# Performance work log

Hardware: AMD Instinct MI355X
Metric: run time of the kernel (lower is better)

Reference implementation:

```python
import jax, jax.numpy as jnp
import numpy as np

TOP_K = 2
EPS = 1e-10


def setup_inputs() -> dict:
    key = jax.random.key(0)
    k1, k2, k3, k4 = jax.random.split(key, 4)
    B, S, H, E = 4, 2048, 1024, 8
    tokens = jax.random.normal(k1, (B, S, H), dtype=jnp.float32)
    router_w = jax.random.normal(k2, (E, H), dtype=jnp.float32) * (1.0 / np.sqrt(H))
    router_b = jax.random.normal(k3, (E,), dtype=jnp.float32) * 0.01
    expert_weights = jax.random.normal(k4, (E, H, H), dtype=jnp.float32) * (1.0 / np.sqrt(H))
    return {"tokens": tokens, "router_w": router_w, "router_b": router_b,
            "expert_weights": expert_weights}


def reference(tokens, router_w, router_b, expert_weights):
    B, S, H = tokens.shape
    E = expert_weights.shape[0]
    # Router (torch Linear: x @ W^T + b)
    logits = jnp.einsum('bsh,eh->bse', tokens, router_w) + router_b  # [B,S,E]
    probs = jax.nn.softmax(logits, axis=-1)
    top_p, top_i = jax.lax.top_k(probs, TOP_K)            # [B,S,K]
    w = top_p / (jnp.sum(top_p, axis=-1, keepdims=True) + EPS)  # normalized weights

    x = tokens.reshape(-1, H)                              # [N,H]
    idx = top_i.reshape(-1, TOP_K)                         # [N,K]
    wf = w.reshape(-1, TOP_K)                              # [N,K]

    # Expert GEMM: compute all experts then gather selected (dense, vectorized
    # equivalent of the sort/pad/grouped-GEMM dispatch; padded rows with
    # original_indices==-1 never contribute to the output).
    y_all = jnp.einsum('nh,ehd->ned', x, expert_weights)   # [N,E,H]
    y_k = jnp.take_along_axis(y_all, idx[:, :, None], axis=1)  # [N,K,H]

    out = jnp.einsum('nk,nkh->nh', wf, y_k)                # weighted combine
    acc = jnp.clip(jnp.sum(wf, axis=-1), EPS, None)        # weight accumulator
    out = (out / acc[:, None]).reshape(B, S, H)

    # epsilon scale tying output to normalized router probs (gradient path)
    scale = 1.0 + jnp.sum(w, axis=-1, keepdims=True) * EPS  # [B,S,1]
    return out * scale
```

## Files before the change

kernel.cpp:

```cpp
#include <hip/hip_runtime.h>
#include <stdint.h>

#define N_TOK 8192
#define H_DIM 1024
#define N_EXP 8
#define GEMM_GRID 1056

typedef __bf16 bf16x8 __attribute__((ext_vector_type(8)));
typedef float floatx4 __attribute__((ext_vector_type(4)));

typedef __attribute__((address_space(1))) void GV;
typedef __attribute__((address_space(3))) void LV;

static __device__ __forceinline__ unsigned short f2b(float f) {
    union { float f; unsigned int i; } v; v.f = f;
    unsigned int u = v.i;
    return (unsigned short)((u + 0x7FFFu + ((u >> 16) & 1u)) >> 16);
}
static __device__ __forceinline__ float b2f(unsigned short u) {
    union { unsigned int i; float f; } v; v.i = ((unsigned int)u) << 16; return v.f;
}

__global__ __launch_bounds__(256) void k_front(
    const float* __restrict__ tokens,
    const float* __restrict__ router_w,
    const float* __restrict__ router_b,
    const float* __restrict__ W,
    int* __restrict__ sel, float* __restrict__ w_arr,
    unsigned short* __restrict__ tokb,
    unsigned short* __restrict__ Bp)
{
    const int t = threadIdx.x;

    if (blockIdx.x >= 2048) {
        const int idx = blockIdx.x - 2048;
        const int kg = idx & 127;
        const int e  = idx >> 7;
        const int d  = t * 4;
        const float* src = W + ((size_t)e * H_DIM + kg * 8) * H_DIM + d;
        float col[8][4];
#pragma unroll
        for (int j = 0; j < 8; ++j) {
            float4 v = *(const float4*)(src + (size_t)j * H_DIM);
            col[j][0] = v.x; col[j][1] = v.y; col[j][2] = v.z; col[j][3] = v.w;
        }
        unsigned short* dst = Bp + ((size_t)(e * 128 + kg) * H_DIM + d) * 8;
#pragma unroll
        for (int k = 0; k < 4; ++k) {
            unsigned short v[8];
#pragma unroll
            for (int j = 0; j < 8; ++j) v[j] = f2b(col[j][k]);
            *(uint4*)(dst + (size_t)k * 8) = *(uint4*)v;
        }
        return;
    }

    const int wave = t >> 6;
    const int lane = t & 63;
    const int n = blockIdx.x * 4 + wave;

    const float* xp = tokens + (size_t)n * H_DIM + lane * 16;
    float x[16];
#pragma unroll
    for (int i = 0; i < 4; ++i) {
        float4 v = *(const float4*)(xp + i * 4);
        x[i * 4 + 0] = v.x; x[i * 4 + 1] = v.y; x[i * 4 + 2] = v.z; x[i * 4 + 3] = v.w;
    }

    {
        unsigned short xb[16];
#pragma unroll
        for (int j = 0; j < 16; ++j) xb[j] = f2b(x[j]);
        unsigned short* dp = tokb + (size_t)n * H_DIM + lane * 16;
        *(uint4*)(dp)     = *(uint4*)(xb);
        *(uint4*)(dp + 8) = *(uint4*)(xb + 8);
    }

    float acc[N_EXP];
#pragma unroll
    for (int e = 0; e < N_EXP; ++e) {
        const float* wp = router_w + e * H_DIM + lane * 16;
        float s = 0.f;
#pragma unroll
        for (int i = 0; i < 4; ++i) {
            float4 v = *(const float4*)(wp + i * 4);
            s += x[i * 4 + 0] * v.x + x[i * 4 + 1] * v.y
               + x[i * 4 + 2] * v.z + x[i * 4 + 3] * v.w;
        }
        acc[e] = s;
    }

#pragma unroll
    for (int e = 0; e < N_EXP; ++e) {
        float a = acc[e];
#pragma unroll
        for (int off = 32; off > 0; off >>= 1) a += __shfl_xor(a, off);
        acc[e] = a;
    }

    if (lane == 0) {
        float lg[N_EXP];
#pragma unroll
        for (int e = 0; e < N_EXP; ++e) lg[e] = acc[e] + router_b[e];
        int e0 = 0;
#pragma unroll
        for (int e = 1; e < N_EXP; ++e) if (lg[e] > lg[e0]) e0 = e;
        int e1 = -1;
#pragma unroll
        for (int e = 0; e < N_EXP; ++e) {
            if (e == e0) continue;
            if (e1 < 0 || lg[e] > lg[e1]) e1 = e;
        }
        float w0 = 1.f / (1.f + __expf(lg[e1] - lg[e0]));
        float w1 = 1.f - w0;
        sel[n] = e0 | (e1 << 4);
        w_arr[n * 2] = w0;
        w_arr[n * 2 + 1] = w1;
    }
}

__global__ __launch_bounds__(256) void k_scan(
    const int* __restrict__ sel, int* __restrict__ cnt, int* __restrict__ bucket)
{
    __shared__ int ssel[N_TOK + N_TOK / 32];
    __shared__ int sc[256];
    const int e = blockIdx.x;
    const int t = threadIdx.x;
#pragma unroll
    for (int i = 0; i < 32; ++i) {
        int n = i * 256 + t;
        ssel[n + (n >> 5)] = sel[n];
    }
    __syncthreads();
    const int base = t * 32;
    int c = 0;
#pragma unroll
    for (int i = 0; i < 32; ++i) {
        int n = base + i;
        int s = ssel[n + (n >> 5)];
        c += ((s & 15) == e) + (((s >> 4) & 15) == e);
    }
    sc[t] = c;
    __syncthreads();
    for (int off = 1; off < 256; off <<= 1) {
        int v = (t >= off) ? sc[t - off] : 0;
        __syncthreads();
        sc[t] += v;
        __syncthreads();
    }
    int pos = sc[t] - c;
    if (t == 255) cnt[e] = sc[255];
#pragma unroll
    for (int i = 0; i < 32; ++i) {
        int n = base + i;
        int s = ssel[n + (n >> 5)];
        if ((s & 15) == e)        bucket[e * N_TOK + pos++] = 2 * n;
        if (((s >> 4) & 15) == e) bucket[e * N_TOK + pos++] = 2 * n + 1;
    }
}

__global__ __launch_bounds__(128, 3) void k_gemm(
    const unsigned short* __restrict__ tokb,
    const unsigned short* __restrict__ Bp,
    const int* __restrict__ cnt, const int* __restrict__ bucket,
    unsigned short* __restrict__ Y)
{
    __shared__ __align__(16) unsigned short Asm[64 * 64];
    __shared__ __align__(16) unsigned short Bsm[8 * 128 * 8];

    const int t = threadIdx.x;
    const int wv = t >> 6, lane = t & 63;
    const int m_lane = lane & 15, quad = lane >> 4;
    const int p_sw = (lane & 7) ^ ((lane >> 3) & 7);

    int cs[N_EXP];
#pragma unroll
    for (int ee = 0; ee < N_EXP; ++ee) cs[ee] = cnt[ee];
    int n_t64 = 0;
#pragma unroll
    for (int ee = 0; ee < N_EXP; ++ee) n_t64 += (cs[ee] + 63) >> 6;
    const int n_it = n_t64 * 8;

    for (int item = blockIdx.x; item < n_it; item += GEMM_GRID) {
        const int t64 = item >> 3;
        const int nt  = item & 7;
        int base = 0, e = 0, mt = 0;
#pragma unroll
        for (int ee = 0; ee < N_EXP; ++ee) {
            int te = (cs[ee] + 63) >> 6;
            if (t64 >= base && t64 < base + te) { e = ee; mt = t64 - base; }
            base += te;
        }
        const int cnt_local = cs[e] - mt * 64;
        const int d0 = nt * 128;
        const int* bk = bucket + e * N_TOK + mt * 64;

        const unsigned short* aptr[4];
#pragma unroll
        for (int i = 0; i < 4; ++i) {
            int r = i * 16 + wv * 8 + (lane >> 3);
            int rid = (r < cnt_local) ? bk[r] : -1;
            int tok = (rid >= 0) ? (rid >> 1) : 0;
            aptr[i] = tokb + (size_t)tok * H_DIM + p_sw * 8;
        }
        const unsigned short* bbase = Bp
            + ((size_t)(e * 128) * H_DIM + d0 + wv * 64 + lane) * 8;

        floatx4 acc[4][4];
#pragma unroll
        for (int i = 0; i < 4; ++i)
#pragma unroll
            for (int j = 0; j < 4; ++j) acc[i][j] = (floatx4){0.f, 0.f, 0.f, 0.f};

        for (int kt = 0; kt < H_DIM / 64; ++kt) {
#pragma unroll
            for (int i = 0; i < 4; ++i)
                __builtin_amdgcn_global_load_lds(
                    (GV*)(aptr[i] + kt * 64),
                    (LV*)(&Asm[i * 1024 + wv * 512]), 16, 0, 0);
#pragma unroll
            for (int i = 0; i < 8; ++i)
                __builtin_amdgcn_global_load_lds(
                    (GV*)(bbase + (size_t)(kt * 8 + i) * (H_DIM * 8)),
                    (LV*)(&Bsm[i * 1024 + wv * 512]), 16, 0, 0);
            __syncthreads();

#pragma unroll
            for (int s = 0; s < 2; ++s) {
                bf16x8 a[4], b[4];
#pragma unroll
                for (int i = 0; i < 4; ++i) {
                    int row = i * 16 + m_lane;
                    a[i] = *(const bf16x8*)&Asm[row * 64 + ((s * 4 + quad) ^ (m_lane & 7)) * 8];
                }
#pragma unroll
                for (int j = 0; j < 4; ++j)
                    b[j] = *(const bf16x8*)&Bsm[((s * 4 + quad) * 128 + wv * 64 + j * 16 + m_lane) * 8];
#pragma unroll
                for (int i = 0; i < 4; ++i)
#pragma unroll
                    for (int j = 0; j < 4; ++j)
                        acc[i][j] = __builtin_amdgcn_mfma_f32_16x16x32_bf16(a[i], b[j], acc[i][j], 0, 0, 0);
            }
            __syncthreads();
        }

#pragma unroll
        for (int i = 0; i < 4; ++i) {
            const int lr_base = i * 16 + quad * 4;
#pragma unroll
            for (int reg = 0; reg < 4; ++reg) {
                const int lr = lr_base + reg;
                const int rid = (lr < cnt_local) ? bk[lr] : -1;
                if (rid >= 0) {
                    unsigned short v[4];
#pragma unroll
                    for (int j = 0; j < 4; ++j) v[j] = f2b(acc[i][j][reg]);
                    *(uint2*)(Y + (size_t)rid * H_DIM + d0 + wv * 64 + m_lane * 4) = *(uint2*)v;
                }
            }
        }
    }
}

__global__ __launch_bounds__(256) void k_combine(
    const unsigned short* __restrict__ Y, const float* __restrict__ w_arr,
    float* __restrict__ out)
{
    __shared__ __align__(16) unsigned short Ys[4 * H_DIM];
    const int t = threadIdx.x;
    const int b = blockIdx.x;
    const int wv = t >> 6, lane = t & 63;
    const unsigned short* src = Y + (size_t)b * 4 * H_DIM;
#pragma unroll
    for (int r = 0; r < 2; ++r) {
        __builtin_amdgcn_global_load_lds(
            (GV*)(src + (size_t)r * 2048 + wv * 512 + lane * 8),
            (LV*)(&Ys[r * 2048 + wv * 512]), 16, 0, 0);
    }
    __syncthreads();

    const int tok = t >> 7;
    const int n = 2 * b + tok;
    const int d0 = (t & 127) * 8;
    const int seg = d0 >> 7;
    const int dseg = d0 & 127;
    const int wc = dseg >> 6;
    const int j  = (dseg >> 4) & 3;
    const int m0 = dseg & 15;
    const int sbase = tok * 2 * H_DIM + seg * 128 + wc * 64 + j;
    const float w0 = w_arr[2 * n], w1 = w_arr[2 * n + 1];

    float o[8];
#pragma unroll
    for (int k = 0; k < 8; ++k) {
        int s = sbase + (m0 + k) * 4;
        o[k] = w0 * b2f(Ys[s]) + w1 * b2f(Ys[s + H_DIM]);
    }
    float4* op = (float4*)(out + (size_t)n * H_DIM + d0);
    op[0] = make_float4(o[0], o[1], o[2], o[3]);
    op[1] = make_float4(o[4], o[5], o[6], o[7]);
}

extern "C" void kernel_launch(void* const* d_in, const int* in_sizes, int n_in,
                              void* d_out, int out_size, void* d_ws, size_t ws_size,
                              hipStream_t stream)
{
    const float* tokens   = (const float*)d_in[0];
    const float* router_w = (const float*)d_in[1];
    const float* router_b = (const float*)d_in[2];
    const float* W        = (const float*)d_in[3];
    float* out = (float*)d_out;

    char* ws = (char*)d_ws;
    int*   cnt    = (int*)(ws);
    int*   sel    = (int*)(ws + 1024);
    float* w_arr  = (float*)(ws + 34816);
    int*   bucket = (int*)(ws + 100352);
    unsigned short* tokb = (unsigned short*)(ws + 362496);
    unsigned short* Bp   = (unsigned short*)(ws + 17139712);
    unsigned short* Y    = (unsigned short*)(ws + 33916928);

    k_front  <<<2048 + 1024, 256, 0, stream>>>(tokens, router_w, router_b, W,
                                               sel, w_arr, tokb, Bp);
    k_scan   <<<N_EXP, 256, 0, stream>>>(sel, cnt, bucket);
    k_gemm   <<<GEMM_GRID, 128, 0, stream>>>(tokb, Bp, cnt, bucket, Y);
    k_combine<<<N_TOK * (H_DIM / 8) / 256, 256, 0, stream>>>(Y, w_arr, out);
}
```

Measured before the change: 202.4 us.

## Enlarge GEMM tiles to 128x128 with 4 waves and XCD-aware tile partitioning

The grouped expert GEMM now uses 256-thread blocks computing 128-row by 128-column tiles, so each A tile is reused across twice as many columns as in the old 64-row tiles with 2 waves. Tiles are split into 8 contiguous ranges selected by blockIdx & 7, so blocks sharing a low-bit index (likely the same XCD) work on adjacent tiles and the same expert weights, which is meant to improve L2 reuse. Bucket row indices are staged in shared memory once per tile instead of being re-read from global memory. The trade-offs are more padding waste per expert with 128-row tiles, an extra barrier per tile, and possible load imbalance across the partitions.

```diff
diff --git a/kernel.cpp b/kernel.cpp
--- a/kernel.cpp
+++ b/kernel.cpp
@@ -4,7 +4,7 @@
 #define N_TOK 8192
 #define H_DIM 1024
 #define N_EXP 8
-#define GEMM_GRID 1056
+#define GEMM_GRID 1024
 
 typedef __bf16 bf16x8 __attribute__((ext_vector_type(8)));
 typedef float floatx4 __attribute__((ext_vector_type(4)));
@@ -159,52 +159,65 @@
     }
 }
 
-__global__ __launch_bounds__(128, 3) void k_gemm(
+__global__ __launch_bounds__(256, 4) void k_gemm(
     const unsigned short* __restrict__ tokb,
     const unsigned short* __restrict__ Bp,
     const int* __restrict__ cnt, const int* __restrict__ bucket,
     unsigned short* __restrict__ Y)
 {
-    __shared__ __align__(16) unsigned short Asm[64 * 64];
+    __shared__ __align__(16) unsigned short Asm[128 * 64];
     __shared__ __align__(16) unsigned short Bsm[8 * 128 * 8];
+    __shared__ int rows[128];
 
     const int t = threadIdx.x;
     const int wv = t >> 6, lane = t & 63;
+    const int w_row = wv >> 1, w_col = wv & 1;
     const int m_lane = lane & 15, quad = lane >> 4;
+    const int r7 = m_lane & 7;
     const int p_sw = (lane & 7) ^ ((lane >> 3) & 7);
 
     int cs[N_EXP];
 #pragma unroll
     for (int ee = 0; ee < N_EXP; ++ee) cs[ee] = cnt[ee];
-    int n_t64 = 0;
-#pragma unroll
-    for (int ee = 0; ee < N_EXP; ++ee) n_t64 += (cs[ee] + 63) >> 6;
-    const int n_it = n_t64 * 8;
-
-    for (int item = blockIdx.x; item < n_it; item += GEMM_GRID) {
-        const int t64 = item >> 3;
-        const int nt  = item & 7;
+    int T = 0;
+#pragma unroll
+    for (int ee = 0; ee < N_EXP; ++ee) T += (cs[ee] + 127) >> 7;
+
+    const int x = blockIdx.x & 7;
+    const int sblk = blockIdx.x >> 3;
+    const int q = T >> 3, r = T & 7;
+    const int tstart = (x < r) ? x * (q + 1) : r * (q + 1) + (x - r) * q;
+    const int tcnt   = (x < r) ? (q + 1) : q;
+    const int nloc   = tcnt * 8;
+
+    for (int l = sblk; l < nloc; l += 128) {
+        const int tile = tstart + (l >> 3);
+        const int nt   = l & 7;
         int base = 0, e = 0, mt = 0;
 #pragma unroll
         for (int ee = 0; ee < N_EXP; ++ee) {
-            int te = (cs[ee] + 63) >> 6;
-            if (t64 >= base && t64 < base + te) { e = ee; mt = t64 - base; }
+            int te = (cs[ee] + 127) >> 7;
+            if (tile >= base && tile < base + te) { e = ee; mt = tile - base; }
             base += te;
         }
-        const int cnt_local = cs[e] - mt * 64;
+        const int cnt_local = cs[e] - mt * 128;
         const int d0 = nt * 128;
-        const int* bk = bucket + e * N_TOK + mt * 64;
+
+        __syncthreads();
+        if (t < 128)
+            rows[t] = (t < cnt_local) ? bucket[e * N_TOK + mt * 128 + t] : -1;
+        __syncthreads();
 
         const unsigned short* aptr[4];
 #pragma unroll
         for (int i = 0; i < 4; ++i) {
-            int r = i * 16 + wv * 8 + (lane >> 3);
-            int rid = (r < cnt_local) ? bk[r] : -1;
+            int rr = i * 32 + wv * 8 + (lane >> 3);
+            int rid = rows[rr];
             int tok = (rid >= 0) ? (rid >> 1) : 0;
             aptr[i] = tokb + (size_t)tok * H_DIM + p_sw * 8;
         }
         const unsigned short* bbase = Bp
-            + ((size_t)(e * 128) * H_DIM + d0 + wv * 64 + lane) * 8;
+            + ((size_t)(e * 128 + (t >> 7)) * H_DIM + d0 + (t & 127)) * 8;
 
         floatx4 acc[4][4];
 #pragma unroll
@@ -214,15 +227,14 @@
 
         for (int kt = 0; kt < H_DIM / 64; ++kt) {
 #pragma unroll
-            for (int i = 0; i < 4; ++i)
+            for (int i = 0; i < 4; ++i) {
                 __builtin_amdgcn_global_load_lds(
                     (GV*)(aptr[i] + kt * 64),
-                    (LV*)(&Asm[i * 1024 + wv * 512]), 16, 0, 0);
-#pragma unroll
-            for (int i = 0; i < 8; ++i)
+                    (LV*)(&Asm[i * 2048 + wv * 512]), 16, 0, 0);
                 __builtin_amdgcn_global_load_lds(
-                    (GV*)(bbase + (size_t)(kt * 8 + i) * (H_DIM * 8)),
-                    (LV*)(&Bsm[i * 1024 + wv * 512]), 16, 0, 0);
+                    (GV*)(bbase + (size_t)i * 16384 + (size_t)kt * 65536),
+                    (LV*)(&Bsm[i * 2048 + wv * 512]), 16, 0, 0);
+            }
             __syncthreads();
 
 #pragma unroll
@@ -230,12 +242,12 @@
                 bf16x8 a[4], b[4];
 #pragma unroll
                 for (int i = 0; i < 4; ++i) {
-                    int row = i * 16 + m_lane;
-                    a[i] = *(const bf16x8*)&Asm[row * 64 + ((s * 4 + quad) ^ (m_lane & 7)) * 8];
+                    int row = w_row * 64 + i * 16 + m_lane;
+                    a[i] = *(const bf16x8*)&Asm[row * 64 + ((s * 4 + quad) ^ r7) * 8];
                 }
 #pragma unroll
                 for (int j = 0; j < 4; ++j)
-                    b[j] = *(const bf16x8*)&Bsm[((s * 4 + quad) * 128 + wv * 64 + j * 16 + m_lane) * 8];
+                    b[j] = *(const bf16x8*)&Bsm[((s * 4 + quad) * 128 + w_col * 64 + j * 16 + m_lane) * 8];
 #pragma unroll
                 for (int i = 0; i < 4; ++i)
 #pragma unroll
@@ -247,16 +259,16 @@
 
 #pragma unroll
         for (int i = 0; i < 4; ++i) {
-            const int lr_base = i * 16 + quad * 4;
+            const int lr_base = w_row * 64 + i * 16 + quad * 4;
 #pragma unroll
             for (int reg = 0; reg < 4; ++reg) {
                 const int lr = lr_base + reg;
-                const int rid = (lr < cnt_local) ? bk[lr] : -1;
+                const int rid = rows[lr];
                 if (rid >= 0) {
                     unsigned short v[4];
 #pragma unroll
                     for (int j = 0; j < 4; ++j) v[j] = f2b(acc[i][j][reg]);
-                    *(uint2*)(Y + (size_t)rid * H_DIM + d0 + wv * 64 + m_lane * 4) = *(uint2*)v;
+                    *(uint2*)(Y + (size_t)rid * H_DIM + d0 + w_col * 64 + m_lane * 4) = *(uint2*)v;
                 }
             }
         }
@@ -324,6 +336,6 @@
     k_front  <<<2048 + 1024, 256, 0, stream>>>(tokens, router_w, router_b, W,
                                                sel, w_arr, tokb, Bp);
     k_scan   <<<N_EXP, 256, 0, stream>>>(sel, cnt, bucket);
-    k_gemm   <<<GEMM_GRID, 128, 0, stream>>>(tokb, Bp, cnt, bucket, Y);
+    k_gemm   <<<GEMM_GRID, 256, 0, stream>>>(tokb, Bp, cnt, bucket, Y);
     k_combine<<<N_TOK * (H_DIM / 8) / 256, 256, 0, stream>>>(Y, w_arr, out);
 }
```

After: 186.3 us. 1.09x faster.
